# Kernel optimization log

Hardware: AMD Instinct MI355X
Metric: run time of the kernel (lower is better)

## Reference

```python
import jax, jax.numpy as jnp
import numpy as np

EPS_COS = 1e-8   # torch F.cosine_similarity eps
EPS_L1 = 1e-12   # torch F.normalize eps


def setup_inputs() -> dict:
    key = jax.random.key(0)
    k1, k2, k3, k4 = jax.random.split(key, 4)
    B, D, C = 32768, 768, 200
    features = jax.random.normal(k1, (B, D), dtype=jnp.float32)
    centers = jax.random.normal(k2, (C, D), dtype=jnp.float32)
    labels = jax.random.randint(k3, (B,), 0, C)
    labelled_or_not = jax.random.randint(k4, (B,), 0, 2).astype(jnp.bool_)
    return {"features": features, "centers": centers, "labels": labels,
            "labelled_or_not": labelled_or_not}


def reference(features, centers, labels, labelled_or_not):
    # cosine similarity: x.y / (max(|x|,eps) * max(|y|,eps))
    fn = features / jnp.maximum(jnp.linalg.norm(features, axis=1, keepdims=True), EPS_COS)
    cn = centers / jnp.maximum(jnp.linalg.norm(centers, axis=1, keepdims=True), EPS_COS)
    cos = jnp.einsum('bd,cd->bc', fn, cn)  # [B, C]

    # per-sample sign logic: label column -> +|cos|, all others -> -|cos|
    a = jnp.abs(cos)
    is_label = jax.nn.one_hot(labels, cos.shape[1], dtype=jnp.bool_)  # [B, C]
    signed = jnp.where(is_label, a, -a)

    # L1 normalize per row (||row||_1 == sum of |cos| regardless of signs)
    l1 = jnp.sum(a, axis=1, keepdims=True)
    normed = signed / jnp.maximum(l1, EPS_L1)

    # only labelled rows contribute (row-wise normalize is independent per row,
    # so masking after is equivalent to boolean-indexing before)
    contrib = jnp.where(labelled_or_not[:, None], normed, 0.0)
    return -jnp.sum(contrib)
```

## Files before the change

kernel.cpp:

```cpp
#include <hip/hip_runtime.h>
#include <hip/hip_bf16.h>

#define NROWS 32768
#define DIMS  768
#define NC    200
#define CPAD  256
#define KSTEP 32
#define NSTEP (DIMS / KSTEP)
#define ROWSB 64
#define LDT   40

typedef __attribute__((ext_vector_type(8))) short short8;
typedef __attribute__((ext_vector_type(4))) float f32x4;

__device__ __forceinline__ short f2bfs(float f) {
  union { float f; unsigned u; } x; x.f = f;
  unsigned u = x.u;
  unsigned r = u + 0x7fffu + ((u >> 16) & 1u);
  return (short)(r >> 16);
}

__global__ __launch_bounds__(256) void prep_centers_k(const float* __restrict__ centers,
                                                      short* __restrict__ cnb2) {
  const int c = blockIdx.x;
  const int tid = threadIdx.x;
  if (c >= NC) {
    for (int d = tid; d < DIMS; d += 256)
      cnb2[(d >> 5) * (CPAD * KSTEP) + c * KSTEP + (d & 31)] = 0;
    return;
  }
  float ssq = 0.f;
  for (int d = tid; d < DIMS; d += 256) {
    float v = centers[c * DIMS + d];
    ssq += v * v;
  }
#pragma unroll
  for (int off = 32; off > 0; off >>= 1) ssq += __shfl_down(ssq, off);
  __shared__ float red[4];
  const int wid = tid >> 6, lane = tid & 63;
  if (lane == 0) red[wid] = ssq;
  __syncthreads();
  const float tot = red[0] + red[1] + red[2] + red[3];
  const float inv = 1.f / fmaxf(sqrtf(tot), 1e-8f);
  for (int d = tid; d < DIMS; d += 256)
    cnb2[(d >> 5) * (CPAD * KSTEP) + c * KSTEP + (d & 31)] =
        f2bfs(centers[c * DIMS + d] * inv);
}

__global__ __launch_bounds__(256) void cos_loss_k(
    const float* __restrict__ feats,
    const short* __restrict__ cnb2,
    const int* __restrict__ labels,
    const int* __restrict__ labelled,
    float* __restrict__ out) {
  const int tid = threadIdx.x;
  const int w = tid >> 6;
  const int lane = tid & 63;
  const int m = lane & 15;
  const int kg = lane >> 4;
  const int rowBase = blockIdx.x * ROWSB;

  __shared__ short As[2][ROWSB][LDT];
  __shared__ short Bs[2][CPAD][LDT];
  __shared__ float invs[ROWSB];
  __shared__ int   labLds[ROWSB];
  __shared__ int   lblLds[ROWSB];
  __shared__ float l1part[4][ROWSB];
  __shared__ float alpart[4][ROWSB];

  if (tid < ROWSB) {
    labLds[tid] = labels[rowBase + tid];
    lblLds[tid] = labelled[rowBase + tid];
  }

  const int arow = tid >> 2;
  const int akoff = (tid & 3) * 8;
  const float* asrc = feats + (size_t)(rowBase + arow) * DIMS + akoff;
  const short* bsrc = cnb2 + tid * KSTEP;

  f32x4 acc[4][4];
#pragma unroll
  for (int mi = 0; mi < 4; ++mi)
#pragma unroll
    for (int ni = 0; ni < 4; ++ni) acc[mi][ni] = (f32x4){0.f, 0.f, 0.f, 0.f};

  float ssq = 0.f;
  float4 pva, pvb;
  short8 pb0, pb1;
  short8 pb2, pb3;

  pva = *(const float4*)(asrc);
  pvb = *(const float4*)(asrc + 4);
  pb0 = *(const short8*)(bsrc + 0);
  pb1 = *(const short8*)(bsrc + 8);
  pb2 = *(const short8*)(bsrc + 16);
  pb3 = *(const short8*)(bsrc + 24);
  {
    ssq += pva.x*pva.x + pva.y*pva.y + pva.z*pva.z + pva.w*pva.w;
    ssq += pvb.x*pvb.x + pvb.y*pvb.y + pvb.z*pvb.z + pvb.w*pvb.w;
    short8 s;
    s[0]=f2bfs(pva.x); s[1]=f2bfs(pva.y); s[2]=f2bfs(pva.z); s[3]=f2bfs(pva.w);
    s[4]=f2bfs(pvb.x); s[5]=f2bfs(pvb.y); s[6]=f2bfs(pvb.z); s[7]=f2bfs(pvb.w);
    *(short8*)(&As[0][arow][akoff]) = s;
    *(short8*)(&Bs[0][tid][0])  = pb0;
    *(short8*)(&Bs[0][tid][8])  = pb1;
    *(short8*)(&Bs[0][tid][16]) = pb2;
    *(short8*)(&Bs[0][tid][24]) = pb3;
  }
  __syncthreads();

#pragma unroll 2
  for (int ks = 0; ks < NSTEP; ++ks) {
    const int cur = ks & 1, nxt = cur ^ 1;
    if (ks < NSTEP - 1) {
      const int k0 = (ks + 1) * KSTEP;
      pva = *(const float4*)(asrc + k0);
      pvb = *(const float4*)(asrc + k0 + 4);
      const short* bs = bsrc + (size_t)(ks + 1) * (CPAD * KSTEP);
      pb0 = *(const short8*)(bs + 0);
      pb1 = *(const short8*)(bs + 8);
      pb2 = *(const short8*)(bs + 16);
      pb3 = *(const short8*)(bs + 24);
    }
    {
      short8 af[4], bf[4];
#pragma unroll
      for (int mi = 0; mi < 4; ++mi)
        af[mi] = *(const short8*)(&As[cur][mi * 16 + m][kg * 8]);
#pragma unroll
      for (int ni = 0; ni < 4; ++ni)
        bf[ni] = *(const short8*)(&Bs[cur][w * 64 + ni * 16 + m][kg * 8]);
#pragma unroll
      for (int mi = 0; mi < 4; ++mi)
#pragma unroll
        for (int ni = 0; ni < 4; ++ni)
          acc[mi][ni] = __builtin_amdgcn_mfma_f32_16x16x32_bf16(af[mi], bf[ni], acc[mi][ni], 0, 0, 0);
    }
    if (ks < NSTEP - 1) {
      ssq += pva.x*pva.x + pva.y*pva.y + pva.z*pva.z + pva.w*pva.w;
      ssq += pvb.x*pvb.x + pvb.y*pvb.y + pvb.z*pvb.z + pvb.w*pvb.w;
      short8 s;
      s[0]=f2bfs(pva.x); s[1]=f2bfs(pva.y); s[2]=f2bfs(pva.z); s[3]=f2bfs(pva.w);
      s[4]=f2bfs(pvb.x); s[5]=f2bfs(pvb.y); s[6]=f2bfs(pvb.z); s[7]=f2bfs(pvb.w);
      *(short8*)(&As[nxt][arow][akoff]) = s;
      *(short8*)(&Bs[nxt][tid][0])  = pb0;
      *(short8*)(&Bs[nxt][tid][8])  = pb1;
      *(short8*)(&Bs[nxt][tid][16]) = pb2;
      *(short8*)(&Bs[nxt][tid][24]) = pb3;
    }
    __syncthreads();
  }

  ssq += __shfl_xor(ssq, 1);
  ssq += __shfl_xor(ssq, 2);
  if ((tid & 3) == 0) invs[arow] = 1.f / fmaxf(sqrtf(ssq), 1e-8f);
  __syncthreads();

#pragma unroll
  for (int mi = 0; mi < 4; ++mi) {
    float l1r[4] = {0.f, 0.f, 0.f, 0.f};
    float alr[4] = {0.f, 0.f, 0.f, 0.f};
    float iv[4];
    int labr[4];
#pragma unroll
    for (int r = 0; r < 4; ++r) {
      const int row = mi * 16 + kg * 4 + r;
      iv[r] = invs[row];
      labr[r] = labLds[row];
    }
#pragma unroll
    for (int ni = 0; ni < 4; ++ni) {
      const int col = w * 64 + ni * 16 + m;
#pragma unroll
      for (int r = 0; r < 4; ++r) {
        const float a = fabsf(acc[mi][ni][r] * iv[r]);
        l1r[r] += a;
        if (col == labr[r]) alr[r] += a;
      }
    }
#pragma unroll
    for (int r = 0; r < 4; ++r) {
#pragma unroll
      for (int off = 1; off < 16; off <<= 1) {
        l1r[r] += __shfl_xor(l1r[r], off);
        alr[r] += __shfl_xor(alr[r], off);
      }
    }
    if (m == 0) {
#pragma unroll
      for (int r = 0; r < 4; ++r) {
        l1part[w][mi * 16 + kg * 4 + r] = l1r[r];
        alpart[w][mi * 16 + kg * 4 + r] = alr[r];
      }
    }
  }
  __syncthreads();

  if (tid < ROWSB) {
    const float L = l1part[0][tid] + l1part[1][tid] + l1part[2][tid] + l1part[3][tid];
    const float A = alpart[0][tid] + alpart[1][tid] + alpart[2][tid] + alpart[3][tid];
    float c = lblLds[tid] ? (L - 2.f * A) / fmaxf(L, 1e-12f) : 0.f;
#pragma unroll
    for (int off = 1; off < 64; off <<= 1) c += __shfl_xor(c, off);
    if (tid == 0) atomicAdd(out, c);
  }
}

extern "C" void kernel_launch(void* const* d_in, const int* in_sizes, int n_in,
                              void* d_out, int out_size, void* d_ws, size_t ws_size,
                              hipStream_t stream) {
  const float* feats = (const float*)d_in[0];
  const float* centers = (const float*)d_in[1];
  const int* labels = (const int*)d_in[2];
  const int* labelled = (const int*)d_in[3];
  float* out = (float*)d_out;
  short* cnb2 = (short*)d_ws;

  hipMemsetAsync(out, 0, sizeof(float) * out_size, stream);
  prep_centers_k<<<CPAD, 256, 0, stream>>>(centers, cnb2);
  cos_loss_k<<<NROWS / ROWSB, 256, 0, stream>>>(feats, cnb2, labels, labelled, out);
}
```

Measured before the change: 41.03 us.

## Load full feature rows to LDS once and stream centers directly from global

```diff
diff --git a/kernel.cpp b/kernel.cpp
--- a/kernel.cpp
+++ b/kernel.cpp
@@ -7,10 +7,11 @@
 #define CPAD  256
 #define KSTEP 32
 #define NSTEP (DIMS / KSTEP)
-#define ROWSB 64
-#define LDT   40
+#define ROWSB 32
+#define LDA   776
 
 typedef __attribute__((ext_vector_type(8))) short short8;
+typedef __attribute__((ext_vector_type(4))) short short4v;
 typedef __attribute__((ext_vector_type(4))) float f32x4;
 
 __device__ __forceinline__ short f2bfs(float f) {
@@ -21,9 +22,11 @@
 }
 
 __global__ __launch_bounds__(256) void prep_centers_k(const float* __restrict__ centers,
-                                                      short* __restrict__ cnb2) {
+                                                      short* __restrict__ cnb2,
+                                                      float* __restrict__ out) {
   const int c = blockIdx.x;
   const int tid = threadIdx.x;
+  if (c == 0 && tid == 0) out[0] = 0.f;
   if (c >= NC) {
     for (int d = tid; d < DIMS; d += 256)
       cnb2[(d >> 5) * (CPAD * KSTEP) + c * KSTEP + (d & 31)] = 0;
@@ -60,8 +63,7 @@
   const int kg = lane >> 4;
   const int rowBase = blockIdx.x * ROWSB;
 
-  __shared__ short As[2][ROWSB][LDT];
-  __shared__ short Bs[2][CPAD][LDT];
+  __shared__ short As[ROWSB][LDA];
   __shared__ float invs[ROWSB];
   __shared__ int   labLds[ROWSB];
   __shared__ int   lblLds[ROWSB];
@@ -73,91 +75,51 @@
     lblLds[tid] = labelled[rowBase + tid];
   }
 
-  const int arow = tid >> 2;
-  const int akoff = (tid & 3) * 8;
-  const float* asrc = feats + (size_t)(rowBase + arow) * DIMS + akoff;
-  const short* bsrc = cnb2 + tid * KSTEP;
+  {
+    const int r = tid >> 3;
+    const int c = tid & 7;
+    const float* src = feats + (size_t)(rowBase + r) * DIMS;
+    float ssq = 0.f;
+#pragma unroll
+    for (int j = 0; j < 24; ++j) {
+      const int col = (c + j * 8) * 4;
+      const float4 v = *(const float4*)(src + col);
+      ssq += v.x * v.x + v.y * v.y + v.z * v.z + v.w * v.w;
+      short4v s4;
+      s4[0] = f2bfs(v.x); s4[1] = f2bfs(v.y); s4[2] = f2bfs(v.z); s4[3] = f2bfs(v.w);
+      *(short4v*)(&As[r][col]) = s4;
+    }
+#pragma unroll
+    for (int off = 1; off < 8; off <<= 1) ssq += __shfl_xor(ssq, off);
+    if (c == 0) invs[r] = 1.f / fmaxf(sqrtf(ssq), 1e-8f);
+  }
+  __syncthreads();
 
-  f32x4 acc[4][4];
+  f32x4 acc[2][4];
 #pragma unroll
-  for (int mi = 0; mi < 4; ++mi)
+  for (int mi = 0; mi < 2; ++mi)
 #pragma unroll
     for (int ni = 0; ni < 4; ++ni) acc[mi][ni] = (f32x4){0.f, 0.f, 0.f, 0.f};
 
-  float ssq = 0.f;
-  float4 pva, pvb;
-  short8 pb0, pb1;
-  short8 pb2, pb3;
+  const short* a0p = &As[m][kg * 8];
+  const short* a1p = &As[16 + m][kg * 8];
+  const short* bp = cnb2 + (size_t)(w * 64 + m) * KSTEP + kg * 8;
 
-  pva = *(const float4*)(asrc);
-  pvb = *(const float4*)(asrc + 4);
-  pb0 = *(const short8*)(bsrc + 0);
-  pb1 = *(const short8*)(bsrc + 8);
-  pb2 = *(const short8*)(bsrc + 16);
-  pb3 = *(const short8*)(bsrc + 24);
-  {
-    ssq += pva.x*pva.x + pva.y*pva.y + pva.z*pva.z + pva.w*pva.w;
-    ssq += pvb.x*pvb.x + pvb.y*pvb.y + pvb.z*pvb.z + pvb.w*pvb.w;
-    short8 s;
-    s[0]=f2bfs(pva.x); s[1]=f2bfs(pva.y); s[2]=f2bfs(pva.z); s[3]=f2bfs(pva.w);
-    s[4]=f2bfs(pvb.x); s[5]=f2bfs(pvb.y); s[6]=f2bfs(pvb.z); s[7]=f2bfs(pvb.w);
-    *(short8*)(&As[0][arow][akoff]) = s;
-    *(short8*)(&Bs[0][tid][0])  = pb0;
-    *(short8*)(&Bs[0][tid][8])  = pb1;
-    *(short8*)(&Bs[0][tid][16]) = pb2;
-    *(short8*)(&Bs[0][tid][24]) = pb3;
-  }
-  __syncthreads();
-
-#pragma unroll 2
+#pragma unroll 4
   for (int ks = 0; ks < NSTEP; ++ks) {
-    const int cur = ks & 1, nxt = cur ^ 1;
-    if (ks < NSTEP - 1) {
-      const int k0 = (ks + 1) * KSTEP;
-      pva = *(const float4*)(asrc + k0);
-      pvb = *(const float4*)(asrc + k0 + 4);
-      const short* bs = bsrc + (size_t)(ks + 1) * (CPAD * KSTEP);
-      pb0 = *(const short8*)(bs + 0);
-      pb1 = *(const short8*)(bs + 8);
-      pb2 = *(const short8*)(bs + 16);
-      pb3 = *(const short8*)(bs + 24);
+    const short8 a0 = *(const short8*)(a0p + ks * KSTEP);
+    const short8 a1 = *(const short8*)(a1p + ks * KSTEP);
+    const short* bs = bp + (size_t)ks * (CPAD * KSTEP);
+#pragma unroll
+    for (int ni = 0; ni < 4; ++ni) {
+      const short8 bf = *(const short8*)(bs + ni * (16 * KSTEP));
+      acc[0][ni] = __builtin_amdgcn_mfma_f32_16x16x32_bf16(a0, bf, acc[0][ni], 0, 0, 0);
+      acc[1][ni] = __builtin_amdgcn_mfma_f32_16x16x32_bf16(a1, bf, acc[1][ni], 0, 0, 0);
     }
-    {
-      short8 af[4], bf[4];
-#pragma unroll
-      for (int mi = 0; mi < 4; ++mi)
-        af[mi] = *(const short8*)(&As[cur][mi * 16 + m][kg * 8]);
-#pragma unroll
-      for (int ni = 0; ni < 4; ++ni)
-        bf[ni] = *(const short8*)(&Bs[cur][w * 64 + ni * 16 + m][kg * 8]);
-#pragma unroll
-      for (int mi = 0; mi < 4; ++mi)
-#pragma unroll
-        for (int ni = 0; ni < 4; ++ni)
-          acc[mi][ni] = __builtin_amdgcn_mfma_f32_16x16x32_bf16(af[mi], bf[ni], acc[mi][ni], 0, 0, 0);
-    }
-    if (ks < NSTEP - 1) {
-      ssq += pva.x*pva.x + pva.y*pva.y + pva.z*pva.z + pva.w*pva.w;
-      ssq += pvb.x*pvb.x + pvb.y*pvb.y + pvb.z*pvb.z + pvb.w*pvb.w;
-      short8 s;
-      s[0]=f2bfs(pva.x); s[1]=f2bfs(pva.y); s[2]=f2bfs(pva.z); s[3]=f2bfs(pva.w);
-      s[4]=f2bfs(pvb.x); s[5]=f2bfs(pvb.y); s[6]=f2bfs(pvb.z); s[7]=f2bfs(pvb.w);
-      *(short8*)(&As[nxt][arow][akoff]) = s;
-      *(short8*)(&Bs[nxt][tid][0])  = pb0;
-      *(short8*)(&Bs[nxt][tid][8])  = pb1;
-      *(short8*)(&Bs[nxt][tid][16]) = pb2;
-      *(short8*)(&Bs[nxt][tid][24]) = pb3;
-    }
-    __syncthreads();
   }
 
-  ssq += __shfl_xor(ssq, 1);
-  ssq += __shfl_xor(ssq, 2);
-  if ((tid & 3) == 0) invs[arow] = 1.f / fmaxf(sqrtf(ssq), 1e-8f);
-  __syncthreads();
-
 #pragma unroll
-  for (int mi = 0; mi < 4; ++mi) {
+  for (int mi = 0; mi < 2; ++mi) {
     float l1r[4] = {0.f, 0.f, 0.f, 0.f};
     float alr[4] = {0.f, 0.f, 0.f, 0.f};
     float iv[4];
@@ -201,7 +163,7 @@
     const float A = alpart[0][tid] + alpart[1][tid] + alpart[2][tid] + alpart[3][tid];
     float c = lblLds[tid] ? (L - 2.f * A) / fmaxf(L, 1e-12f) : 0.f;
 #pragma unroll
-    for (int off = 1; off < 64; off <<= 1) c += __shfl_xor(c, off);
+    for (int off = 1; off < 32; off <<= 1) c += __shfl_xor(c, off);
     if (tid == 0) atomicAdd(out, c);
   }
 }
@@ -216,7 +178,6 @@
   float* out = (float*)d_out;
   short* cnb2 = (short*)d_ws;
 
-  hipMemsetAsync(out, 0, sizeof(float) * out_size, stream);
-  prep_centers_k<<<CPAD, 256, 0, stream>>>(centers, cnb2);
+  prep_centers_k<<<CPAD, 256, 0, stream>>>(centers, cnb2, out);
   cos_loss_k<<<NROWS / ROWSB, 256, 0, stream>>>(feats, cnb2, labels, labelled, out);
 }
```

Result: slower. 56.13 us (+36.8%).

## Swizzle LDS tiles with XOR, use packed bf16 conversion, drop memset launch

Applied to the files above, without the earlier changes.

```diff
diff --git a/kernel.cpp b/kernel.cpp
--- a/kernel.cpp
+++ b/kernel.cpp
@@ -8,22 +8,22 @@
 #define KSTEP 32
 #define NSTEP (DIMS / KSTEP)
 #define ROWSB 64
-#define LDT   40
 
 typedef __attribute__((ext_vector_type(8))) short short8;
 typedef __attribute__((ext_vector_type(4))) float f32x4;
 
-__device__ __forceinline__ short f2bfs(float f) {
-  union { float f; unsigned u; } x; x.f = f;
-  unsigned u = x.u;
-  unsigned r = u + 0x7fffu + ((u >> 16) & 1u);
-  return (short)(r >> 16);
+__device__ __forceinline__ unsigned pk_bf16(float lo, float hi) {
+  union { __hip_bfloat162 h; unsigned u; } c;
+  c.h = __float22bfloat162_rn(make_float2(lo, hi));
+  return c.u;
 }
 
 __global__ __launch_bounds__(256) void prep_centers_k(const float* __restrict__ centers,
-                                                      short* __restrict__ cnb2) {
+                                                      short* __restrict__ cnb2,
+                                                      float* __restrict__ out) {
   const int c = blockIdx.x;
   const int tid = threadIdx.x;
+  if (c == 0 && tid == 0) out[0] = 0.f;
   if (c >= NC) {
     for (int d = tid; d < DIMS; d += 256)
       cnb2[(d >> 5) * (CPAD * KSTEP) + c * KSTEP + (d & 31)] = 0;
@@ -42,9 +42,12 @@
   __syncthreads();
   const float tot = red[0] + red[1] + red[2] + red[3];
   const float inv = 1.f / fmaxf(sqrtf(tot), 1e-8f);
-  for (int d = tid; d < DIMS; d += 256)
-    cnb2[(d >> 5) * (CPAD * KSTEP) + c * KSTEP + (d & 31)] =
-        f2bfs(centers[c * DIMS + d] * inv);
+  for (int d = tid; d < DIMS; d += 256) {
+    const float v = centers[c * DIMS + d] * inv;
+    union { __hip_bfloat16 h; short s; } cv;
+    cv.h = __float2bfloat16(v);
+    cnb2[(d >> 5) * (CPAD * KSTEP) + c * KSTEP + (d & 31)] = cv.s;
+  }
 }
 
 __global__ __launch_bounds__(256) void cos_loss_k(
@@ -58,10 +61,11 @@
   const int lane = tid & 63;
   const int m = lane & 15;
   const int kg = lane >> 4;
+  const int swzf = (m >> 1) & 3;
   const int rowBase = blockIdx.x * ROWSB;
 
-  __shared__ short As[2][ROWSB][LDT];
-  __shared__ short Bs[2][CPAD][LDT];
+  __shared__ short As[2][ROWSB][32];
+  __shared__ short Bs[2][CPAD][32];
   __shared__ float invs[ROWSB];
   __shared__ int   labLds[ROWSB];
   __shared__ int   lblLds[ROWSB];
@@ -74,9 +78,14 @@
   }
 
   const int arow = tid >> 2;
-  const int akoff = (tid & 3) * 8;
-  const float* asrc = feats + (size_t)(rowBase + arow) * DIMS + akoff;
-  const short* bsrc = cnb2 + tid * KSTEP;
+  const int akg  = tid & 3;
+  const int aswz = (arow >> 1) & 3;
+  const float* asrc = feats + (size_t)(rowBase + arow) * DIMS + akg * 8;
+  short* adst0 = &As[0][arow][(akg ^ aswz) * 8];
+  short* adst1 = &As[1][arow][(akg ^ aswz) * 8];
+  const int bcol = tid;
+  const int bswz = (bcol >> 1) & 3;
+  const short* bsrc = cnb2 + bcol * KSTEP;
 
   f32x4 acc[4][4];
 #pragma unroll
@@ -85,51 +94,50 @@
     for (int ni = 0; ni < 4; ++ni) acc[mi][ni] = (f32x4){0.f, 0.f, 0.f, 0.f};
 
   float ssq = 0.f;
-  float4 pva, pvb;
-  short8 pb0, pb1;
-  short8 pb2, pb3;
-
-  pva = *(const float4*)(asrc);
-  pvb = *(const float4*)(asrc + 4);
-  pb0 = *(const short8*)(bsrc + 0);
-  pb1 = *(const short8*)(bsrc + 8);
-  pb2 = *(const short8*)(bsrc + 16);
-  pb3 = *(const short8*)(bsrc + 24);
+
   {
-    ssq += pva.x*pva.x + pva.y*pva.y + pva.z*pva.z + pva.w*pva.w;
-    ssq += pvb.x*pvb.x + pvb.y*pvb.y + pvb.z*pvb.z + pvb.w*pvb.w;
-    short8 s;
-    s[0]=f2bfs(pva.x); s[1]=f2bfs(pva.y); s[2]=f2bfs(pva.z); s[3]=f2bfs(pva.w);
-    s[4]=f2bfs(pvb.x); s[5]=f2bfs(pvb.y); s[6]=f2bfs(pvb.z); s[7]=f2bfs(pvb.w);
-    *(short8*)(&As[0][arow][akoff]) = s;
-    *(short8*)(&Bs[0][tid][0])  = pb0;
-    *(short8*)(&Bs[0][tid][8])  = pb1;
-    *(short8*)(&Bs[0][tid][16]) = pb2;
-    *(short8*)(&Bs[0][tid][24]) = pb3;
+    const float4 va = *(const float4*)(asrc);
+    const float4 vb = *(const float4*)(asrc + 4);
+    ssq += va.x*va.x + va.y*va.y + va.z*va.z + va.w*va.w;
+    ssq += vb.x*vb.x + vb.y*vb.y + vb.z*vb.z + vb.w*vb.w;
+    union { short8 s; unsigned u[4]; } p;
+    p.u[0] = pk_bf16(va.x, va.y); p.u[1] = pk_bf16(va.z, va.w);
+    p.u[2] = pk_bf16(vb.x, vb.y); p.u[3] = pk_bf16(vb.z, vb.w);
+    *(short8*)adst0 = p.s;
+    const short8 b0 = *(const short8*)(bsrc + 0);
+    const short8 b1 = *(const short8*)(bsrc + 8);
+    const short8 b2 = *(const short8*)(bsrc + 16);
+    const short8 b3 = *(const short8*)(bsrc + 24);
+    *(short8*)(&Bs[0][bcol][((0 ^ bswz)) * 8]) = b0;
+    *(short8*)(&Bs[0][bcol][((1 ^ bswz)) * 8]) = b1;
+    *(short8*)(&Bs[0][bcol][((2 ^ bswz)) * 8]) = b2;
+    *(short8*)(&Bs[0][bcol][((3 ^ bswz)) * 8]) = b3;
   }
   __syncthreads();
 
 #pragma unroll 2
   for (int ks = 0; ks < NSTEP; ++ks) {
     const int cur = ks & 1, nxt = cur ^ 1;
+    float4 va, vb;
+    short8 b0, b1, b2, b3;
     if (ks < NSTEP - 1) {
-      const int k0 = (ks + 1) * KSTEP;
-      pva = *(const float4*)(asrc + k0);
-      pvb = *(const float4*)(asrc + k0 + 4);
-      const short* bs = bsrc + (size_t)(ks + 1) * (CPAD * KSTEP);
-      pb0 = *(const short8*)(bs + 0);
-      pb1 = *(const short8*)(bs + 8);
-      pb2 = *(const short8*)(bs + 16);
-      pb3 = *(const short8*)(bs + 24);
+      const float* ap = asrc + (ks + 1) * KSTEP;
+      va = *(const float4*)(ap);
+      vb = *(const float4*)(ap + 4);
+      const short* bp = bsrc + (size_t)(ks + 1) * (CPAD * KSTEP);
+      b0 = *(const short8*)(bp + 0);
+      b1 = *(const short8*)(bp + 8);
+      b2 = *(const short8*)(bp + 16);
+      b3 = *(const short8*)(bp + 24);
     }
     {
       short8 af[4], bf[4];
 #pragma unroll
       for (int mi = 0; mi < 4; ++mi)
-        af[mi] = *(const short8*)(&As[cur][mi * 16 + m][kg * 8]);
+        af[mi] = *(const short8*)(&As[cur][mi * 16 + m][((kg ^ swzf)) * 8]);
 #pragma unroll
       for (int ni = 0; ni < 4; ++ni)
-        bf[ni] = *(const short8*)(&Bs[cur][w * 64 + ni * 16 + m][kg * 8]);
+        bf[ni] = *(const short8*)(&Bs[cur][w * 64 + ni * 16 + m][((kg ^ swzf)) * 8]);
 #pragma unroll
       for (int mi = 0; mi < 4; ++mi)
 #pragma unroll
@@ -137,16 +145,16 @@
           acc[mi][ni] = __builtin_amdgcn_mfma_f32_16x16x32_bf16(af[mi], bf[ni], acc[mi][ni], 0, 0, 0);
     }
     if (ks < NSTEP - 1) {
-      ssq += pva.x*pva.x + pva.y*pva.y + pva.z*pva.z + pva.w*pva.w;
-      ssq += pvb.x*pvb.x + pvb.y*pvb.y + pvb.z*pvb.z + pvb.w*pvb.w;
-      short8 s;
-      s[0]=f2bfs(pva.x); s[1]=f2bfs(pva.y); s[2]=f2bfs(pva.z); s[3]=f2bfs(pva.w);
-      s[4]=f2bfs(pvb.x); s[5]=f2bfs(pvb.y); s[6]=f2bfs(pvb.z); s[7]=f2bfs(pvb.w);
-      *(short8*)(&As[nxt][arow][akoff]) = s;
-      *(short8*)(&Bs[nxt][tid][0])  = pb0;
-      *(short8*)(&Bs[nxt][tid][8])  = pb1;
-      *(short8*)(&Bs[nxt][tid][16]) = pb2;
-      *(short8*)(&Bs[nxt][tid][24]) = pb3;
+      ssq += va.x*va.x + va.y*va.y + va.z*va.z + va.w*va.w;
+      ssq += vb.x*vb.x + vb.y*vb.y + vb.z*vb.z + vb.w*vb.w;
+      union { short8 s; unsigned u[4]; } p;
+      p.u[0] = pk_bf16(va.x, va.y); p.u[1] = pk_bf16(va.z, va.w);
+      p.u[2] = pk_bf16(vb.x, vb.y); p.u[3] = pk_bf16(vb.z, vb.w);
+      *(short8*)(nxt ? adst1 : adst0) = p.s;
+      *(short8*)(&Bs[nxt][bcol][((0 ^ bswz)) * 8]) = b0;
+      *(short8*)(&Bs[nxt][bcol][((1 ^ bswz)) * 8]) = b1;
+      *(short8*)(&Bs[nxt][bcol][((2 ^ bswz)) * 8]) = b2;
+      *(short8*)(&Bs[nxt][bcol][((3 ^ bswz)) * 8]) = b3;
     }
     __syncthreads();
   }
@@ -216,7 +224,6 @@
   float* out = (float*)d_out;
   short* cnb2 = (short*)d_ws;
 
-  hipMemsetAsync(out, 0, sizeof(float) * out_size, stream);
-  prep_centers_k<<<CPAD, 256, 0, stream>>>(centers, cnb2);
+  prep_centers_k<<<CPAD, 256, 0, stream>>>(centers, cnb2, out);
   cos_loss_k<<<NROWS / ROWSB, 256, 0, stream>>>(feats, cnb2, labels, labelled, out);
 }
```

New measurement: 38.01 us. 7.3% less time.
